# Performance work log

Measured on AMD Instinct MI355X. Metric: run time of the kernel, lower is better.

The kernel has to match this reference:

```python
import jax, jax.numpy as jnp
import numpy as np

TOP_K = 2
NEG_INF = float('-inf')


def setup_inputs() -> dict:
    key = jax.random.key(0)
    kx, kw = jax.random.split(key)
    B, S, D, E = 4, 4096, 2048, 64
    x = jax.random.normal(kx, (B, S, D), dtype=jnp.float32)
    W = jax.random.normal(kw, (E, D), dtype=jnp.float32) * (1.0 / np.sqrt(D))
    b = jnp.zeros((E,), dtype=jnp.float32)
    return {"x": x, "W": W, "b": b}


def reference(x, W, b):
    # logits: [B, S, E] -- small linear gate
    logits = jnp.einsum('bsd,ed->bse', x, W) + b
    B, S, E = logits.shape
    # top-k over experts
    topk_vals, topk_idx = jax.lax.top_k(logits, TOP_K)  # [B,S,K]
    # scatter top-k logits into a -inf filled tensor
    flat_vals = topk_vals.reshape(-1, TOP_K)            # [T, K]
    flat_idx = topk_idx.reshape(-1, TOP_K)              # [T, K]
    T = flat_idx.shape[0]
    sparse = jnp.full((T, E), NEG_INF, dtype=logits.dtype)
    sparse = sparse.at[jnp.arange(T)[:, None], flat_idx].set(flat_vals)
    # softmax over experts; -inf entries become exactly 0
    router_output = jax.nn.softmax(sparse, axis=-1).reshape(B, S, E)
    return router_output, topk_idx
```

## Files before the change

### kernel.cpp

```cpp
#include <hip/hip_runtime.h>
#include <math.h>


#define RD 2048
#define RE 64
#define TB 16
#define NCQ 8

typedef __attribute__((ext_vector_type(8))) short bf16x8;
typedef __attribute__((ext_vector_type(4))) float f32x4;
typedef __attribute__((ext_vector_type(4))) unsigned int u32x4;

__device__ __forceinline__ unsigned short f2b(float f) {
    unsigned int u = __float_as_uint(f);
    unsigned int r = ((u >> 16) & 1u) + 0x7fffu;
    return (unsigned short)((u + r) >> 16);
}
__device__ __forceinline__ float b2f(unsigned short h) {
    return __uint_as_float(((unsigned int)h) << 16);
}

__device__ __forceinline__ void cvt8(const f32x4 a, const f32x4 bq,
                                     unsigned int* h, unsigned int* l,
                                     unsigned int* l2) {
    float v[8] = {a.x, a.y, a.z, a.w, bq.x, bq.y, bq.z, bq.w};
#pragma unroll
    for (int j = 0; j < 4; ++j) {
        const float a0 = v[2 * j], a1 = v[2 * j + 1];
        const unsigned short h0 = f2b(a0); const float r0 = a0 - b2f(h0);
        const unsigned short h1 = f2b(a1); const float r1 = a1 - b2f(h1);
        const unsigned short m0 = f2b(r0); const float s0 = r0 - b2f(m0);
        const unsigned short m1 = f2b(r1); const float s1 = r1 - b2f(m1);
        const unsigned short q0 = f2b(s0);
        const unsigned short q1 = f2b(s1);
        h[j]  = (unsigned int)h0 | ((unsigned int)h1 << 16);
        l[j]  = (unsigned int)m0 | ((unsigned int)m1 << 16);
        l2[j] = (unsigned int)q0 | ((unsigned int)q1 << 16);
    }
}

__global__ __launch_bounds__(256) void wprep_kernel(
    const float* __restrict__ W, unsigned int* __restrict__ WB)
{
    const int ks = blockIdx.x;
    const int et = threadIdx.x >> 6;
    const int lane = threadIdx.x & 63;
    const int e = et * 16 + (lane & 15);
    const int k0 = ks * 32 + (lane >> 4) * 8;
    const float* src = W + (size_t)e * RD + k0;
    const f32x4 a = *(const f32x4*)(src);
    const f32x4 bq = *(const f32x4*)(src + 4);
    unsigned int h[4], l[4], l2[4];
    cvt8(a, bq, h, l, l2);
    unsigned int* dst = WB + (size_t)((ks * 4 + et) * 3) * 256 + lane * 4;
    *(u32x4*)(dst)       = *(u32x4*)h;
    *(u32x4*)(dst + 256) = *(u32x4*)l;
    *(u32x4*)(dst + 512) = *(u32x4*)l2;
}

#define SIXMFMA(AH, AL, AQ, ACC, WP) do {                                  \
    const bf16x8 Bh_ = *(const bf16x8*)(WP);                               \
    const bf16x8 Bl_ = *(const bf16x8*)((WP) + 256);                       \
    const bf16x8 Bq_ = *(const bf16x8*)((WP) + 512);                       \
    ACC = __builtin_amdgcn_mfma_f32_16x16x32_bf16(AH, Bh_, ACC, 0, 0, 0);  \
    ACC = __builtin_amdgcn_mfma_f32_16x16x32_bf16(AH, Bl_, ACC, 0, 0, 0);  \
    ACC = __builtin_amdgcn_mfma_f32_16x16x32_bf16(AL, Bh_, ACC, 0, 0, 0);  \
    ACC = __builtin_amdgcn_mfma_f32_16x16x32_bf16(AL, Bl_, ACC, 0, 0, 0);  \
    ACC = __builtin_amdgcn_mfma_f32_16x16x32_bf16(AH, Bq_, ACC, 0, 0, 0);  \
    ACC = __builtin_amdgcn_mfma_f32_16x16x32_bf16(AQ, Bh_, ACC, 0, 0, 0);  \
} while (0)

__global__ __launch_bounds__(256, 4) void topk_router_kernel(
    const float* __restrict__ x,
    const unsigned int* __restrict__ WB,
    const float* __restrict__ b,
    float* __restrict__ out_router,
    float* __restrict__ out_idx,
    int total_tokens)
{
    const int tid = threadIdx.x;
    const int lane = tid & 63;
    const int wq = __builtin_amdgcn_readfirstlane(tid >> 6);
    const int tok0 = blockIdx.x * TB;

    __shared__ __align__(16) float PS[4][TB][68];

    const int tmax = total_tokens - 1;
    const int row = min(tok0 + (lane & 15), tmax);
    const float* ga = x + (size_t)row * RD + wq * (RD / 4) + (lane >> 4) * 8;

    f32x4 acc0 = {0.f, 0.f, 0.f, 0.f};
    f32x4 acc1 = {0.f, 0.f, 0.f, 0.f};
    f32x4 acc2 = {0.f, 0.f, 0.f, 0.f};
    f32x4 acc3 = {0.f, 0.f, 0.f, 0.f};

    f32x4 p0 = *(const f32x4*)(ga + 0);
    f32x4 p1 = *(const f32x4*)(ga + 4);
    f32x4 p2 = *(const f32x4*)(ga + 32);
    f32x4 p3 = *(const f32x4*)(ga + 36);

#pragma unroll 1
    for (int c = 0; c < NCQ; ++c) {
        const int cn = (c + 1 < NCQ) ? (c + 1) : 0;
        const float* gn = ga + (size_t)cn * 64;
        const f32x4 n0 = *(const f32x4*)(gn + 0);
        const f32x4 n1 = *(const f32x4*)(gn + 4);
        const f32x4 n2 = *(const f32x4*)(gn + 32);
        const f32x4 n3 = *(const f32x4*)(gn + 36);

        unsigned int h0[4], l0[4], q0[4], h1[4], l1[4], q1[4];
        cvt8(p0, p1, h0, l0, q0);
        cvt8(p2, p3, h1, l1, q1);
        const bf16x8 A0h = *(const bf16x8*)h0;
        const bf16x8 A0l = *(const bf16x8*)l0;
        const bf16x8 A0q = *(const bf16x8*)q0;
        const bf16x8 A1h = *(const bf16x8*)h1;
        const bf16x8 A1l = *(const bf16x8*)l1;
        const bf16x8 A1q = *(const bf16x8*)q1;

        const int ksg0 = wq * 16 + c * 2;
        const unsigned int* wp00 = WB + (size_t)((ksg0 * 4 + 0) * 3) * 256 + lane * 4;
        const unsigned int* wp01 = WB + (size_t)((ksg0 * 4 + 1) * 3) * 256 + lane * 4;
        const unsigned int* wp02 = WB + (size_t)((ksg0 * 4 + 2) * 3) * 256 + lane * 4;
        const unsigned int* wp03 = WB + (size_t)((ksg0 * 4 + 3) * 3) * 256 + lane * 4;
        SIXMFMA(A0h, A0l, A0q, acc0, wp00);
        SIXMFMA(A0h, A0l, A0q, acc1, wp01);
        SIXMFMA(A0h, A0l, A0q, acc2, wp02);
        SIXMFMA(A0h, A0l, A0q, acc3, wp03);

        const int ksg1 = ksg0 + 1;
        const unsigned int* wp10 = WB + (size_t)((ksg1 * 4 + 0) * 3) * 256 + lane * 4;
        const unsigned int* wp11 = WB + (size_t)((ksg1 * 4 + 1) * 3) * 256 + lane * 4;
        const unsigned int* wp12 = WB + (size_t)((ksg1 * 4 + 2) * 3) * 256 + lane * 4;
        const unsigned int* wp13 = WB + (size_t)((ksg1 * 4 + 3) * 3) * 256 + lane * 4;
        SIXMFMA(A1h, A1l, A1q, acc0, wp10);
        SIXMFMA(A1h, A1l, A1q, acc1, wp11);
        SIXMFMA(A1h, A1l, A1q, acc2, wp12);
        SIXMFMA(A1h, A1l, A1q, acc3, wp13);

        p0 = n0; p1 = n1; p2 = n2; p3 = n3;
    }

#pragma unroll
    for (int r = 0; r < 4; ++r) {
        const int t = (lane >> 4) * 4 + r;
        PS[wq][t][0 * 16 + (lane & 15)] = acc0[r];
        PS[wq][t][1 * 16 + (lane & 15)] = acc1[r];
        PS[wq][t][2 * 16 + (lane & 15)] = acc2[r];
        PS[wq][t][3 * 16 + (lane & 15)] = acc3[r];
    }
    __syncthreads();

    const double bias = (double)b[lane];

#pragma unroll 1
    for (int i = 0; i < 4; ++i) {
        const int t = wq * 4 + i;
        const int token = tok0 + t;
        const double v = (double)PS[0][t][lane] + (double)PS[1][t][lane]
                       + (double)PS[2][t][lane] + (double)PS[3][t][lane] + bias;

        double bestv = v;
        int besti = lane;
#pragma unroll
        for (int off = 32; off > 0; off >>= 1) {
            double ov = __shfl_xor(bestv, off, 64);
            int oi = __shfl_xor(besti, off, 64);
            if (ov > bestv || (ov == bestv && oi < besti)) { bestv = ov; besti = oi; }
        }

        double v2 = (lane == besti) ? -INFINITY : v;
        double best2v = v2;
        int best2i = lane;
#pragma unroll
        for (int off = 32; off > 0; off >>= 1) {
            double ov = __shfl_xor(best2v, off, 64);
            int oi = __shfl_xor(best2i, off, 64);
            if (ov > best2v || (ov == best2v && oi < best2i)) { best2v = ov; best2i = oi; }
        }

        const float e2 = expf((float)(best2v - bestv));
        const float denom = 1.0f + e2;
        const float p1v = 1.0f / denom;
        const float p2v = e2 / denom;

        if (token < total_tokens) {
            float outv = 0.0f;
            if (lane == besti) outv = p1v;
            else if (lane == best2i) outv = p2v;
            out_router[(size_t)token * RE + lane] = outv;
            if (lane == 0) {
                out_idx[(size_t)token * 2 + 0] = (float)besti;
                out_idx[(size_t)token * 2 + 1] = (float)best2i;
            }
        }
    }
}

extern "C" void kernel_launch(void* const* d_in, const int* in_sizes, int n_in,
                              void* d_out, int out_size, void* d_ws, size_t ws_size,
                              hipStream_t stream) {
    const float* x = (const float*)d_in[0];
    const float* W = (const float*)d_in[1];
    const float* b = (const float*)d_in[2];

    const int E = in_sizes[2];
    const int D = in_sizes[1] / E;
    const int T = in_sizes[0] / D;
    (void)E; (void)D;

    unsigned int* WB = (unsigned int*)d_ws;
    float* out_router = (float*)d_out;
    float* out_idx = out_router + (size_t)T * RE;

    wprep_kernel<<<64, 256, 0, stream>>>(W, WB);

    const int grid = (T + TB - 1) / TB;
    topk_router_kernel<<<grid, 256, 0, stream>>>(x, WB, b, out_router, out_idx, T);
}
```

Before: 59.33 us.

## Process 32 tokens per block so each W fragment load feeds two row tiles

Doubles the token tile per block from 16 to 32. Each wave now computes two 16-row MFMA tiles that share every loaded W hi/lo/q fragment, which halves W traffic per token and halves the number of blocks. Launch bounds drop to 2 blocks per SM to make room for the doubled accumulators and prefetch registers. It also adds an odd fp64 accumulation of the first expert group that only fires on the last iteration. That path is effectively a copy plus a cast, adds register pressure, and looks like leftover or confused code.

```diff
diff --git a/kernel.cpp b/kernel.cpp
--- a/kernel.cpp
+++ b/kernel.cpp
@@ -4,7 +4,7 @@
 
 #define RD 2048
 #define RE 64
-#define TB 16
+#define TB 32
 #define NCQ 8
 
 typedef __attribute__((ext_vector_type(8))) short bf16x8;
@@ -58,19 +58,25 @@
     *(u32x4*)(dst + 512) = *(u32x4*)l2;
 }
 
-#define SIXMFMA(AH, AL, AQ, ACC, WP) do {                                  \
+#define TWELVE(AH0, AL0, AQ0, AH1, AL1, AQ1, ACC0, ACC1, WP) do {          \
     const bf16x8 Bh_ = *(const bf16x8*)(WP);                               \
     const bf16x8 Bl_ = *(const bf16x8*)((WP) + 256);                       \
     const bf16x8 Bq_ = *(const bf16x8*)((WP) + 512);                       \
-    ACC = __builtin_amdgcn_mfma_f32_16x16x32_bf16(AH, Bh_, ACC, 0, 0, 0);  \
-    ACC = __builtin_amdgcn_mfma_f32_16x16x32_bf16(AH, Bl_, ACC, 0, 0, 0);  \
-    ACC = __builtin_amdgcn_mfma_f32_16x16x32_bf16(AL, Bh_, ACC, 0, 0, 0);  \
-    ACC = __builtin_amdgcn_mfma_f32_16x16x32_bf16(AL, Bl_, ACC, 0, 0, 0);  \
-    ACC = __builtin_amdgcn_mfma_f32_16x16x32_bf16(AH, Bq_, ACC, 0, 0, 0);  \
-    ACC = __builtin_amdgcn_mfma_f32_16x16x32_bf16(AQ, Bh_, ACC, 0, 0, 0);  \
+    ACC0 = __builtin_amdgcn_mfma_f32_16x16x32_bf16(AH0, Bh_, ACC0, 0, 0, 0); \
+    ACC0 = __builtin_amdgcn_mfma_f32_16x16x32_bf16(AH0, Bl_, ACC0, 0, 0, 0); \
+    ACC0 = __builtin_amdgcn_mfma_f32_16x16x32_bf16(AL0, Bh_, ACC0, 0, 0, 0); \
+    ACC0 = __builtin_amdgcn_mfma_f32_16x16x32_bf16(AL0, Bl_, ACC0, 0, 0, 0); \
+    ACC0 = __builtin_amdgcn_mfma_f32_16x16x32_bf16(AH0, Bq_, ACC0, 0, 0, 0); \
+    ACC0 = __builtin_amdgcn_mfma_f32_16x16x32_bf16(AQ0, Bh_, ACC0, 0, 0, 0); \
+    ACC1 = __builtin_amdgcn_mfma_f32_16x16x32_bf16(AH1, Bh_, ACC1, 0, 0, 0); \
+    ACC1 = __builtin_amdgcn_mfma_f32_16x16x32_bf16(AH1, Bl_, ACC1, 0, 0, 0); \
+    ACC1 = __builtin_amdgcn_mfma_f32_16x16x32_bf16(AL1, Bh_, ACC1, 0, 0, 0); \
+    ACC1 = __builtin_amdgcn_mfma_f32_16x16x32_bf16(AL1, Bl_, ACC1, 0, 0, 0); \
+    ACC1 = __builtin_amdgcn_mfma_f32_16x16x32_bf16(AH1, Bq_, ACC1, 0, 0, 0); \
+    ACC1 = __builtin_amdgcn_mfma_f32_16x16x32_bf16(AQ1, Bh_, ACC1, 0, 0, 0); \
 } while (0)
 
-__global__ __launch_bounds__(256, 4) void topk_router_kernel(
+__global__ __launch_bounds__(256, 2) void topk_router_kernel(
     const float* __restrict__ x,
     const unsigned int* __restrict__ WB,
     const float* __restrict__ b,
@@ -86,76 +92,100 @@
     __shared__ __align__(16) float PS[4][TB][68];
 
     const int tmax = total_tokens - 1;
-    const int row = min(tok0 + (lane & 15), tmax);
-    const float* ga = x + (size_t)row * RD + wq * (RD / 4) + (lane >> 4) * 8;
-
-    f32x4 acc0 = {0.f, 0.f, 0.f, 0.f};
-    f32x4 acc1 = {0.f, 0.f, 0.f, 0.f};
-    f32x4 acc2 = {0.f, 0.f, 0.f, 0.f};
-    f32x4 acc3 = {0.f, 0.f, 0.f, 0.f};
-
-    f32x4 p0 = *(const f32x4*)(ga + 0);
-    f32x4 p1 = *(const f32x4*)(ga + 4);
-    f32x4 p2 = *(const f32x4*)(ga + 32);
-    f32x4 p3 = *(const f32x4*)(ga + 36);
+    const int row0 = min(tok0 + (lane & 15), tmax);
+    const int row1 = min(tok0 + 16 + (lane & 15), tmax);
+    const float* ga0 = x + (size_t)row0 * RD + wq * (RD / 4) + (lane >> 4) * 8;
+    const float* ga1 = x + (size_t)row1 * RD + wq * (RD / 4) + (lane >> 4) * 8;
+
+    f32x4 aA0 = {0.f,0.f,0.f,0.f}, aA1 = {0.f,0.f,0.f,0.f};
+    f32x4 aA2 = {0.f,0.f,0.f,0.f}, aA3 = {0.f,0.f,0.f,0.f};
+    f32x4 aB0 = {0.f,0.f,0.f,0.f}, aB1 = {0.f,0.f,0.f,0.f};
+    f32x4 aB2 = {0.f,0.f,0.f,0.f}, aB3 = {0.f,0.f,0.f,0.f};
+
+    f32x4 p00 = *(const f32x4*)(ga0 + 0);
+    f32x4 p01 = *(const f32x4*)(ga0 + 4);
+    f32x4 p02 = *(const f32x4*)(ga0 + 32);
+    f32x4 p03 = *(const f32x4*)(ga0 + 36);
+    f32x4 p10 = *(const f32x4*)(ga1 + 0);
+    f32x4 p11 = *(const f32x4*)(ga1 + 4);
+    f32x4 p12 = *(const f32x4*)(ga1 + 32);
+    f32x4 p13 = *(const f32x4*)(ga1 + 36);
+
+    double acc64A[4] = {0.0, 0.0, 0.0, 0.0};
+    double acc64B[4] = {0.0, 0.0, 0.0, 0.0};
 
 #pragma unroll 1
     for (int c = 0; c < NCQ; ++c) {
         const int cn = (c + 1 < NCQ) ? (c + 1) : 0;
-        const float* gn = ga + (size_t)cn * 64;
-        const f32x4 n0 = *(const f32x4*)(gn + 0);
-        const f32x4 n1 = *(const f32x4*)(gn + 4);
-        const f32x4 n2 = *(const f32x4*)(gn + 32);
-        const f32x4 n3 = *(const f32x4*)(gn + 36);
-
-        unsigned int h0[4], l0[4], q0[4], h1[4], l1[4], q1[4];
-        cvt8(p0, p1, h0, l0, q0);
-        cvt8(p2, p3, h1, l1, q1);
-        const bf16x8 A0h = *(const bf16x8*)h0;
-        const bf16x8 A0l = *(const bf16x8*)l0;
-        const bf16x8 A0q = *(const bf16x8*)q0;
-        const bf16x8 A1h = *(const bf16x8*)h1;
-        const bf16x8 A1l = *(const bf16x8*)l1;
-        const bf16x8 A1q = *(const bf16x8*)q1;
+        const float* g0n = ga0 + (size_t)cn * 64;
+        const float* g1n = ga1 + (size_t)cn * 64;
+        const f32x4 n00 = *(const f32x4*)(g0n + 0);
+        const f32x4 n01 = *(const f32x4*)(g0n + 4);
+        const f32x4 n02 = *(const f32x4*)(g0n + 32);
+        const f32x4 n03 = *(const f32x4*)(g0n + 36);
+        const f32x4 n10 = *(const f32x4*)(g1n + 0);
+        const f32x4 n11 = *(const f32x4*)(g1n + 4);
+        const f32x4 n12 = *(const f32x4*)(g1n + 32);
+        const f32x4 n13 = *(const f32x4*)(g1n + 36);
+
+        unsigned int h00[4], l00[4], q00[4], h01[4], l01[4], q01[4];
+        unsigned int h10[4], l10[4], q10[4], h11[4], l11[4], q11[4];
+        cvt8(p00, p01, h00, l00, q00);
+        cvt8(p02, p03, h01, l01, q01);
+        cvt8(p10, p11, h10, l10, q10);
+        cvt8(p12, p13, h11, l11, q11);
+        const bf16x8 A00h = *(const bf16x8*)h00, A00l = *(const bf16x8*)l00,
+                     A00q = *(const bf16x8*)q00;
+        const bf16x8 A01h = *(const bf16x8*)h01, A01l = *(const bf16x8*)l01,
+                     A01q = *(const bf16x8*)q01;
+        const bf16x8 A10h = *(const bf16x8*)h10, A10l = *(const bf16x8*)l10,
+                     A10q = *(const bf16x8*)q10;
+        const bf16x8 A11h = *(const bf16x8*)h11, A11l = *(const bf16x8*)l11,
+                     A11q = *(const bf16x8*)q11;
 
         const int ksg0 = wq * 16 + c * 2;
-        const unsigned int* wp00 = WB + (size_t)((ksg0 * 4 + 0) * 3) * 256 + lane * 4;
-        const unsigned int* wp01 = WB + (size_t)((ksg0 * 4 + 1) * 3) * 256 + lane * 4;
-        const unsigned int* wp02 = WB + (size_t)((ksg0 * 4 + 2) * 3) * 256 + lane * 4;
-        const unsigned int* wp03 = WB + (size_t)((ksg0 * 4 + 3) * 3) * 256 + lane * 4;
-        SIXMFMA(A0h, A0l, A0q, acc0, wp00);
-        SIXMFMA(A0h, A0l, A0q, acc1, wp01);
-        SIXMFMA(A0h, A0l, A0q, acc2, wp02);
-        SIXMFMA(A0h, A0l, A0q, acc3, wp03);
-
-        const int ksg1 = ksg0 + 1;
-        const unsigned int* wp10 = WB + (size_t)((ksg1 * 4 + 0) * 3) * 256 + lane * 4;
-        const unsigned int* wp11 = WB + (size_t)((ksg1 * 4 + 1) * 3) * 256 + lane * 4;
-        const unsigned int* wp12 = WB + (size_t)((ksg1 * 4 + 2) * 3) * 256 + lane * 4;
-        const unsigned int* wp13 = WB + (size_t)((ksg1 * 4 + 3) * 3) * 256 + lane * 4;
-        SIXMFMA(A1h, A1l, A1q, acc0, wp10);
-        SIXMFMA(A1h, A1l, A1q, acc1, wp11);
-        SIXMFMA(A1h, A1l, A1q, acc2, wp12);
-        SIXMFMA(A1h, A1l, A1q, acc3, wp13);
-
-        p0 = n0; p1 = n1; p2 = n2; p3 = n3;
+        const unsigned int* w0 = WB + (size_t)(ksg0 * 4 * 3) * 256 + lane * 4;
+        TWELVE(A00h, A00l, A00q, A10h, A10l, A10q, aA0, aB0, w0 + 0 * 768);
+        TWELVE(A00h, A00l, A00q, A10h, A10l, A10q, aA1, aB1, w0 + 1 * 768);
+        TWELVE(A00h, A00l, A00q, A10h, A10l, A10q, aA2, aB2, w0 + 2 * 768);
+        TWELVE(A00h, A00l, A00q, A10h, A10l, A10q, aA3, aB3, w0 + 3 * 768);
+
+        const unsigned int* w1 = w0 + 4 * 768;
+        TWELVE(A01h, A01l, A01q, A11h, A11l, A11q, aA0, aB0, w1 + 0 * 768);
+        TWELVE(A01h, A01l, A01q, A11h, A11l, A11q, aA1, aB1, w1 + 1 * 768);
+        TWELVE(A01h, A01l, A01q, A11h, A11l, A11q, aA2, aB2, w1 + 2 * 768);
+        TWELVE(A01h, A01l, A01q, A11h, A11l, A11q, aA3, aB3, w1 + 3 * 768);
+
+        if ((c & 7) == 7) {
+            acc64A[0] += (double)aA0.x; acc64A[1] += (double)aA0.y;
+            acc64A[2] += (double)aA0.z; acc64A[3] += (double)aA0.w;
+            acc64B[0] += (double)aB0.x; acc64B[1] += (double)aB0.y;
+            acc64B[2] += (double)aB0.z; acc64B[3] += (double)aB0.w;
+        }
+
+        p00 = n00; p01 = n01; p02 = n02; p03 = n03;
+        p10 = n10; p11 = n11; p12 = n12; p13 = n13;
     }
 
 #pragma unroll
     for (int r = 0; r < 4; ++r) {
         const int t = (lane >> 4) * 4 + r;
-        PS[wq][t][0 * 16 + (lane & 15)] = acc0[r];
-        PS[wq][t][1 * 16 + (lane & 15)] = acc1[r];
-        PS[wq][t][2 * 16 + (lane & 15)] = acc2[r];
-        PS[wq][t][3 * 16 + (lane & 15)] = acc3[r];
+        PS[wq][t][0 * 16 + (lane & 15)] = (float)acc64A[r];
+        PS[wq][t][1 * 16 + (lane & 15)] = aA1[r];
+        PS[wq][t][2 * 16 + (lane & 15)] = aA2[r];
+        PS[wq][t][3 * 16 + (lane & 15)] = aA3[r];
+        PS[wq][16 + t][0 * 16 + (lane & 15)] = (float)acc64B[r];
+        PS[wq][16 + t][1 * 16 + (lane & 15)] = aB1[r];
+        PS[wq][16 + t][2 * 16 + (lane & 15)] = aB2[r];
+        PS[wq][16 + t][3 * 16 + (lane & 15)] = aB3[r];
     }
     __syncthreads();
 
     const double bias = (double)b[lane];
 
 #pragma unroll 1
-    for (int i = 0; i < 4; ++i) {
-        const int t = wq * 4 + i;
+    for (int i = 0; i < 8; ++i) {
+        const int t = wq * 8 + i;
         const int token = tok0 + t;
         const double v = (double)PS[0][t][lane] + (double)PS[1][t][lane]
                        + (double)PS[2][t][lane] + (double)PS[3][t][lane] + bias;
```

After: 58.52 us. No clear change (-1.4%).
